# Kernel tuning notes

Hardware: AMD Instinct MI355X
Metric: run time of the kernel (lower is better)

## Reference

```python
import jax, jax.numpy as jnp
import numpy as np

RANK = 16
RATIO_1 = 0.01
RATIO_2 = 0.01
N_POWER_ITERS = 2  # randomized SVD power iterations (torch.svd_lowrank-style)


def _lowrank_V(A, rank, key):
    """Randomized low-rank right factor V (n, rank) of A (m, n), a la svd_lowrank."""
    m, n = A.shape
    omega = jax.random.normal(key, (n, rank), dtype=A.dtype)
    Q, _ = jnp.linalg.qr(A @ omega)              # (m, rank)
    for _ in range(N_POWER_ITERS):
        Z, _ = jnp.linalg.qr(A.T @ Q)            # (n, rank)
        Q, _ = jnp.linalg.qr(A @ Z)              # (m, rank)
    B = Q.T @ A                                  # (rank, n) small
    _, _, Vt = jnp.linalg.svd(B, full_matrices=False)
    return Vt.T                                  # (n, rank), orthonormal cols


def _get_statistics(x, ratio):
    # threshold such that ~ratio fraction of |x| entries are outliers
    return jnp.quantile(jnp.abs(x), 1.0 - ratio)


def _compress(x, thresh, rank, key):
    d = x.shape[-1]
    x2d = x.reshape(-1, d)                       # (M, D)
    outliers = jnp.where(jnp.abs(x2d) > thresh, x2d, jnp.zeros((), x2d.dtype))
    residual = x2d - outliers
    R = _lowrank_V(residual, rank, key)          # (D, rank)
    L = residual @ R                             # (M, rank)
    Rinv = R.T                                   # orthonormal cols -> pinv = R^T
    return outliers, L, R, Rinv


def reference(x1, x2):
    # Hadamard product (the module's returned value)
    result = x1 * x2
    # iteration == 0 path: compute statistics and run SVD compression
    out1 = _get_statistics(x1, RATIO_1)
    out2 = _get_statistics(x2, RATIO_2)
    k = jax.random.key(42)
    k1, k2 = jax.random.split(k)
    _, _, R1, Rinv1 = _compress(x1, out1, RANK, k1)
    _, _, R2, Rinv2 = _compress(x2, out2, RANK, k2)
    return (result, out1, R1, Rinv1, out2, R2, Rinv2)


def setup_inputs() -> dict:
    key = jax.random.key(0)
    k1, k2 = jax.random.split(key)
    x1 = jax.random.normal(k1, (4, 2048, 4096), dtype=jnp.float32)
    x2 = jax.random.normal(k2, (4, 2048, 4096), dtype=jnp.float32)
    return {"x1": x1, "x2": x2}
```

## Files before the change

kernel.cpp:

```cpp
#include <hip/hip_runtime.h>
#include <cstdint>
#include <cstddef>


#define DEV __device__ __forceinline__

typedef float nfloat4 __attribute__((ext_vector_type(4)));

constexpr long long NTOT = 33554432LL;
constexpr unsigned long long KSEL = 33218888ULL;
constexpr uint32_t WLO = 0x40100000u;

constexpr long long OUT_T1  = 33554432LL;
constexpr long long OUT_R1  = 33554433LL;
constexpr long long OUT_RI1 = 33619969LL;
constexpr long long OUT_T2  = 33685505LL;
constexpr long long OUT_R2  = 33685506LL;
constexpr long long OUT_RI2 = 33751042LL;

constexpr size_t OFF_WPART  = 0;
constexpr size_t OFF_BPART  = 0;
constexpr size_t OFF_FB     = 4194304;
constexpr size_t OFF_CNT    = 6291456;
constexpr size_t OFF_GF     = 6291472;
constexpr size_t ZERO_BASE  = OFF_FB;
constexpr size_t ZERO_FLOATS= 2099216;
constexpr size_t OFF_CHIST  = 6291456;
constexpr size_t OFF_COARSE = 8388608;
constexpr size_t OFF_SEGS   = 8392704;
constexpr size_t OFF_SELR   = 8394752;
constexpr size_t OFF_TSEL   = 8394768;
constexpr size_t OFF_OMT    = 8394784;
constexpr size_t OFF_BIGY   = 8525856;
constexpr size_t OFF_BIGQ   = 8788000;
constexpr size_t OFF_ZT     = 9050144;
constexpr size_t OFF_QQR    = 9181216;
constexpr size_t OFF_TMAT   = 9312288;
constexpr size_t OFF_GRAMP  = 9443360;
constexpr size_t OFF_S      = 9476128;
constexpr size_t OFF_QTOP   = 9476640;
constexpr size_t OFF_RG     = 9477152;
constexpr size_t OFF_VTL    = 9477664;

DEV float frcp_(float x){ return __builtin_amdgcn_rcpf(x); }
DEV float fdivf_(float a, float b){ return a * __builtin_amdgcn_rcpf(b); }
DEV float fsqrtf_(float x){ return __builtin_amdgcn_sqrtf(x); }

#define TFR(a,b,r) { a += b; b = (b << r) | (b >> (32 - r)); b ^= a; }

DEV void d_threefry(uint32_t k0, uint32_t k1, uint32_t x0, uint32_t x1,
                    uint32_t& o0, uint32_t& o1){
  uint32_t ks2 = k0 ^ k1 ^ 0x1BD11BDAu;
  x0 += k0; x1 += k1;
  TFR(x0,x1,13) TFR(x0,x1,15) TFR(x0,x1,26) TFR(x0,x1,6)
  x0 += k1; x1 += ks2 + 1u;
  TFR(x0,x1,17) TFR(x0,x1,29) TFR(x0,x1,16) TFR(x0,x1,24)
  x0 += ks2; x1 += k0 + 2u;
  TFR(x0,x1,13) TFR(x0,x1,15) TFR(x0,x1,26) TFR(x0,x1,6)
  x0 += k0; x1 += k1 + 3u;
  TFR(x0,x1,17) TFR(x0,x1,29) TFR(x0,x1,16) TFR(x0,x1,24)
  x0 += k1; x1 += ks2 + 4u;
  TFR(x0,x1,13) TFR(x0,x1,15) TFR(x0,x1,26) TFR(x0,x1,6)
  x0 += ks2; x1 += k0 + 5u;
  o0 = x0; o1 = x1;
}

static void h_threefry(uint32_t k0, uint32_t k1, uint32_t x0, uint32_t x1,
                       uint32_t& o0, uint32_t& o1){
  uint32_t ks2 = k0 ^ k1 ^ 0x1BD11BDAu;
  x0 += k0; x1 += k1;
  TFR(x0,x1,13) TFR(x0,x1,15) TFR(x0,x1,26) TFR(x0,x1,6)
  x0 += k1; x1 += ks2 + 1u;
  TFR(x0,x1,17) TFR(x0,x1,29) TFR(x0,x1,16) TFR(x0,x1,24)
  x0 += ks2; x1 += k0 + 2u;
  TFR(x0,x1,13) TFR(x0,x1,15) TFR(x0,x1,26) TFR(x0,x1,6)
  x0 += k0; x1 += k1 + 3u;
  TFR(x0,x1,17) TFR(x0,x1,29) TFR(x0,x1,16) TFR(x0,x1,24)
  x0 += k1; x1 += ks2 + 4u;
  TFR(x0,x1,13) TFR(x0,x1,15) TFR(x0,x1,26) TFR(x0,x1,6)
  x0 += ks2; x1 += k0 + 5u;
  o0 = x0; o1 = x1;
}

DEV float erfinv_f32(float x){
  float w = -log1pf(-x*x);
  float p;
  if (w < 5.0f){
    w -= 2.5f;
    p = 2.81022636e-08f;
    p = fmaf(p, w, 3.43273939e-07f);
    p = fmaf(p, w, -3.5233877e-06f);
    p = fmaf(p, w, -4.39150654e-06f);
    p = fmaf(p, w, 0.00021858087f);
    p = fmaf(p, w, -0.00125372503f);
    p = fmaf(p, w, -0.00417768164f);
    p = fmaf(p, w, 0.246640727f);
    p = fmaf(p, w, 1.50140941f);
  } else {
    w = sqrtf(w) - 3.0f;
    p = -0.000200214257f;
    p = fmaf(p, w, 0.000100950558f);
    p = fmaf(p, w, 0.00134934322f);
    p = fmaf(p, w, -0.00367342844f);
    p = fmaf(p, w, 0.00573950773f);
    p = fmaf(p, w, -0.0076224613f);
    p = fmaf(p, w, 0.00943887047f);
    p = fmaf(p, w, 1.00167406f);
    p = fmaf(p, w, 2.83297682f);
  }
  return p * x;
}

DEV float lapy2f(float x, float y){
  float xa = fabsf(x), ya = fabsf(y);
  float w = fmaxf(xa, ya), z = fminf(xa, ya);
  if (z == 0.f) return w;
  float q = z * frcp_(w);
  return w * fsqrtf_(1.f + q*q);
}

DEV void slartg_(float f, float g, float& c, float& s, float& r){
  if (g == 0.f){ c = 1.f; s = 0.f; r = f; }
  else if (f == 0.f){ c = 0.f; s = copysignf(1.f, g); r = fabsf(g); }
  else {
    float d = fsqrtf_(f*f + g*g);
    float rd = frcp_(d);
    c = fabsf(f) * rd;
    r = copysignf(d, f);
    s = g * copysignf(rd, f);
// ... 168 lines not shown
  ps[threadIdx.x] = s;
  __syncthreads();
  if (threadIdx.x == 0){
    unsigned long long K = KSEL, cum = cnt[ty];
    int valid = 0, sbin = 0, rank = 0;
    if (K >= cum){
      int g = 0;
      for (; g < 256; g++){ if (cum + ps[g] > K) break; cum += ps[g]; }
      if (g < 256){
        for (int j = 0; j < 8; j++){
          uint32_t c = H[g*8 + j];
          if (cum + c > K){ sbin = g*8 + j; rank = (int)(K - cum); valid = 1; break; }
          cum += c;
        }
      }
    }
    selr[0] = sbin; selr[1] = rank; selr[2] = valid;
  }
}

__global__ __launch_bounds__(256) void k_fine(const float* __restrict__ x1,
    const float* __restrict__ x2, float* __restrict__ ws){
  int ty = blockIdx.y;
  const int* selr = (const int*)(ws + OFF_SELR) + ty*4;
  if (!selr[2]) return;
  uint32_t g = (uint32_t)selr[0];
  __shared__ uint32_t lh[1024];
  for (int i = threadIdx.x; i < 1024; i += 256) lh[i] = 0u;
  __syncthreads();
  const float4* x4 = (const float4*)(ty ? x2 : x1);
  long long n4 = NTOT/4;
  long long stride = (long long)gridDim.x * 256;
  for (long long i = (long long)blockIdx.x*256 + threadIdx.x; i < n4; i += stride){
    float4 a = x4[i];
    uint32_t dd;
    dd = (__float_as_uint(a.x)&0x7fffffffu) - WLO;
    if ((dd>>10) == g) atomicAdd(&lh[dd & 1023u], 1u);
    dd = (__float_as_uint(a.y)&0x7fffffffu) - WLO;
    if ((dd>>10) == g) atomicAdd(&lh[dd & 1023u], 1u);
    dd = (__float_as_uint(a.z)&0x7fffffffu) - WLO;
    if ((dd>>10) == g) atomicAdd(&lh[dd & 1023u], 1u);
    dd = (__float_as_uint(a.w)&0x7fffffffu) - WLO;
    if ((dd>>10) == g) atomicAdd(&lh[dd & 1023u], 1u);
  }
  __syncthreads();
  uint32_t* gf = (uint32_t*)(ws + OFF_GF) + (size_t)ty*1024;
  for (int i = threadIdx.x; i < 1024; i += 256){
    uint32_t v = lh[i];
    if (v) atomicAdd(&gf[i], v);
  }
}

__global__ __launch_bounds__(256) void k_fine_sel(float* __restrict__ ws,
    float* __restrict__ out){
  int ty = blockIdx.x;
  const int* selr = (const int*)(ws + OFF_SELR) + ty*4;
  if (!selr[2]) return;
  const uint32_t* gf = (const uint32_t*)(ws + OFF_GF) + (size_t)ty*1024;
  __shared__ uint32_t sh[1024];
  __shared__ uint32_t ps[256];
  int t = threadIdx.x;
  for (int k = 0; k < 4; k++) sh[k*256 + t] = gf[k*256 + t];
  __syncthreads();
  ps[t] = sh[4*t] + sh[4*t+1] + sh[4*t+2] + sh[4*t+3];
  __syncthreads();
  if (t == 0){
    uint32_t K = (uint32_t)selr[1];
    uint32_t cum = 0; int q = 0;
    for (; q < 256; q++){ if (cum + ps[q] > K) break; cum += ps[q]; }
    if (q > 255) q = 255;
    int f = q*4 + 3;
    for (int jj = 0; jj < 4; jj++){
      uint32_t c = sh[q*4 + jj];
      if (cum + c > K){ f = q*4 + jj; break; }
      cum += c;
    }
    uint32_t bits = WLO + (((uint32_t)selr[0]) << 10) + (uint32_t)f;
    float th = __uint_as_float(bits);
    ws[OFF_TSEL + ty] = th;
    out[ty ? OUT_T2 : OUT_T1] = th;
  }
}

__global__ __launch_bounds__(256) void k_hist_fb(const float* __restrict__ x1,
    const float* __restrict__ x2, float* __restrict__ ws){
  const int* selr = (const int*)(ws + OFF_SELR);
  if (selr[2] && selr[4 + 2]) return;
  __shared__ uint32_t lh[2][4][2048];
  for (int i = threadIdx.x; i < 2*4*2048; i += 256) (&lh[0][0][0])[i] = 0u;
  __syncthreads();
  int rep = threadIdx.x & 3;
  const float4* a4 = (const float4*)x1;
  const float4* b4 = (const float4*)x2;
  long long n4 = NTOT/4;
  long long stride = (long long)gridDim.x * 256;
  for (long long i = (long long)blockIdx.x*256 + threadIdx.x; i < n4; i += stride){
    float4 a = a4[i], b = b4[i];
    uint32_t u;
    u = __float_as_uint(a.x)&0x7fffffffu; atomicAdd(&lh[0][rep][u>>20], 1u);
    u = __float_as_uint(a.y)&0x7fffffffu; atomicAdd(&lh[0][rep][u>>20], 1u);
    u = __float_as_uint(a.z)&0x7fffffffu; atomicAdd(&lh[0][rep][u>>20], 1u);
    u = __float_as_uint(a.w)&0x7fffffffu; atomicAdd(&lh[0][rep][u>>20], 1u);
    u = __float_as_uint(b.x)&0x7fffffffu; atomicAdd(&lh[1][rep][u>>20], 1u);
    u = __float_as_uint(b.y)&0x7fffffffu; atomicAdd(&lh[1][rep][u>>20], 1u);
    u = __float_as_uint(b.z)&0x7fffffffu; atomicAdd(&lh[1][rep][u>>20], 1u);
    u = __float_as_uint(b.w)&0x7fffffffu; atomicAdd(&lh[1][rep][u>>20], 1u);
  }
  __syncthreads();
  uint32_t* ch = (uint32_t*)(ws + OFF_CHIST);
  for (int i = threadIdx.x; i < 2048; i += 256){
    uint32_t c0 = lh[0][0][i] + lh[0][1][i] + lh[0][2][i] + lh[0][3][i];
    uint32_t c1 = lh[1][0][i] + lh[1][1][i] + lh[1][2][i] + lh[1][3][i];
    ch[((size_t)blockIdx.x*2 + 0)*2048 + i] = c0;
    ch[((size_t)blockIdx.x*2 + 1)*2048 + i] = c1;
  }
}

__global__ __launch_bounds__(256) void k_coarse_red(float* __restrict__ ws){
  int ty = blockIdx.y;
  if (((const int*)(ws + OFF_SELR))[ty*4 + 2]) return;
  const uint32_t* ch = (const uint32_t*)(ws + OFF_CHIST);
  uint32_t* h = (uint32_t*)(ws + OFF_COARSE) + ty*2048;
  int bin = blockIdx.x*128 + (threadIdx.x & 127);
  int half = threadIdx.x >> 7;
  uint32_t s = 0;
  for (int p = half*256; p < half*256 + 256; p++)
    s += ch[((size_t)p*2 + ty)*2048 + bin];
  __shared__ uint32_t sh[256];
  sh[threadIdx.x] = s;
  __syncthreads();
  if (threadIdx.x < 128) h[bin] = sh[threadIdx.x] + sh[threadIdx.x + 128];
}

__global__ __launch_bounds__(256) void k_coarse_scan(float* __restrict__ ws){
  int ty = blockIdx.x;
  int* selr = (int*)(ws + OFF_SELR) + ty*4;
  if (selr[2]) return;
  const uint32_t* h = (const uint32_t*)(ws + OFF_COARSE) + ty*2048;
  __shared__ unsigned long long ps[256];
  unsigned long long s = 0;
  for (int j = 0; j < 8; j++) s += h[threadIdx.x*8 + j];
  ps[threadIdx.x] = s;
  __syncthreads();
  if (threadIdx.x == 0){
    unsigned long long cum = 0, K = KSEL;
    int g = 0;
    for (; g < 256; g++){ if (cum + ps[g] > K) break; cum += ps[g]; }
    if (g > 255) g = 255;
    int bin = 2047;
    for (int j = 0; j < 8; j++){
      uint32_t c = h[g*8 + j];
      if (cum + c > K){ bin = g*8 + j; break; }
      cum += c;
    }
    selr[0] = bin;
    selr[1] = (int)(K - cum);
  }
}

__global__ __launch_bounds__(256) void k_fine_fb(const float* __restrict__ x1,
    const float* __restrict__ x2, float* __restrict__ ws){
  int ty = blockIdx.y;
  const int* selr = (const int*)(ws + OFF_SELR) + ty*4;
  if (selr[2]) return;
  const float4* x4 = (const float4*)(ty ? x2 : x1);
  uint32_t bin = (uint32_t)selr[0];
  uint32_t* f = (uint32_t*)(ws + OFF_FB) + ((size_t)ty<<20);
  long long n4 = NTOT/4;
  long long stride = (long long)gridDim.x * 256;
  for (long long i = (long long)blockIdx.x*256 + threadIdx.x; i < n4; i += stride){
    float4 a = x4[i];
    uint32_t u;
    u = __float_as_uint(a.x)&0x7fffffffu; if ((u>>20)==bin) atomicAdd(&f[u&0xFFFFFu],1u);
    u = __float_as_uint(a.y)&0x7fffffffu; if ((u>>20)==bin) atomicAdd(&f[u&0xFFFFFu],1u);
    u = __float_as_uint(a.z)&0x7fffffffu; if ((u>>20)==bin) atomicAdd(&f[u&0xFFFFFu],1u);
    u = __float_as_uint(a.w)&0x7fffffffu; if ((u>>20)==bin) atomicAdd(&f[u&0xFFFFFu],1u);
  }
}

__global__ __launch_bounds__(256) void k_seg_sum(float* __restrict__ ws){
  int ty = blockIdx.y;
  const int* selr = (const int*)(ws + OFF_SELR) + ty*4;
  if (selr[2]) return;
  const uint32_t* f = (const uint32_t*)(ws + OFF_FB) + ((size_t)ty<<20);
  uint32_t* segs = (uint32_t*)(ws + OFF_SEGS) + ty*1024;
  uint32_t s = 0;
  int base = blockIdx.x*1024;
  for (int k = 0; k < 4; k++) s += f[base + k*256 + threadIdx.x];
  __shared__ uint32_t sh[256];
  sh[threadIdx.x] = s;
  __syncthreads();
  for (int off = 128; off > 0; off >>= 1){
    if (threadIdx.x < off) sh[threadIdx.x] += sh[threadIdx.x + off];
    __syncthreads();
  }
  if (threadIdx.x == 0) segs[blockIdx.x] = sh[0];
}

__global__ __launch_bounds__(256) void k_fine_scan2(float* __restrict__ ws, float* __restrict__ out){
  int ty = blockIdx.x;
  const int* selr = (const int*)(ws + OFF_SELR) + ty*4;
  if (selr[2]) return;
  const uint32_t* f = (const uint32_t*)(ws + OFF_FB) + ((size_t)ty<<20);
  const uint32_t* segs = (const uint32_t*)(ws + OFF_SEGS) + ty*1024;
  __shared__ uint32_t sh[1024];
  __shared__ uint32_t ps[256];
  __shared__ int gsel; __shared__ uint32_t csel;
  int t = threadIdx.x;
  uint32_t K = (uint32_t)selr[1];
  for (int k = 0; k < 4; k++) sh[k*256 + t] = segs[k*256 + t];
  __syncthreads();
  ps[t] = sh[4*t] + sh[4*t+1] + sh[4*t+2] + sh[4*t+3];
  __syncthreads();
  if (t == 0){
    uint32_t cum = 0; int q = 0;
    for (; q < 256; q++){ if (cum + ps[q] > K) break; cum += ps[q]; }
    if (q > 255) q = 255;
    int g = q*4;
    for (int j = 0; j < 4; j++){
      uint32_t c = sh[q*4 + j];
      if (cum + c > K){ g = q*4 + j; break; }
      cum += c;
      if (j == 3) g = q*4 + 3;
    }
    gsel = g; csel = cum;
  }
  __syncthreads();
  int g = gsel;
  for (int k = 0; k < 4; k++) sh[k*256 + t] = f[(size_t)g*1024 + k*256 + t];
  __syncthreads();
  ps[t] = sh[4*t] + sh[4*t+1] + sh[4*t+2] + sh[4*t+3];
  __syncthreads();
  if (t == 0){
    uint32_t cum = csel; int q = 0;
    for (; q < 256; q++){ if (cum + ps[q] > K) break; cum += ps[q]; }
    if (q > 255) q = 255;
    int j = q*4 + 3;
    for (int jj = 0; jj < 4; jj++){
      uint32_t c = sh[q*4 + jj];
      if (cum + c > K){ j = q*4 + jj; break; }
      cum += c;
    }
    uint32_t bits = (((uint32_t)selr[0])<<20) | (uint32_t)((g*1024 + j) & 0xFFFFF);
    float th = __uint_as_float(bits);
    ws[OFF_TSEL + ty] = th;
    out[ty ? OUT_T2 : OUT_T1] = th;
  }
}

__global__ __launch_bounds__(256) void k_omega(uint32_t a0, uint32_t a1,
    uint32_t b0, uint32_t b1, float* __restrict__ ws){
  int ty = blockIdx.y;
  uint32_t k0 = ty ? b0 : a0, k1 = ty ? b1 : a1;
  int i = blockIdx.x*256 + threadIdx.x;
  uint32_t o0, o1;
  d_threefry(k0, k1, 0u, (uint32_t)i, o0, o1);
  uint32_t bits = o0 ^ o1;
  float fr = __uint_as_float((bits >> 9) | 0x3f800000u) - 1.0f;
  const float lo = -0.99999994f;
  float u = fr * 2.0f + lo;
  u = fmaxf(lo, u);
  float v = 1.41421356237f * erfinv_f32(u);
  int row = i >> 4, col = i & 15;
  ws[OFF_OMT + (size_t)ty*65536 + (size_t)col*4096 + row] = v;
}

__global__ __launch_bounds__(256) void k_atype(const float* __restrict__ x1,
    const float* __restrict__ x2, float* __restrict__ ws, size_t wtOff){
  int ty = blockIdx.y;
  const float* x = ty ? x2 : x1;
  const float* wt = ws + wtOff + (size_t)ty*65536;
  float* Y = ws + OFF_BIGY + (size_t)ty*131072;
  float t = ws[OFF_TSEL + ty];
  int wave = threadIdx.x >> 6, lane = threadIdx.x & 63;
  __shared__ __align__(16) float wts[16][256];
  __shared__ float outs[16][16];
  float acc[4][16];
  #pragma unroll
  for (int r = 0; r < 4; r++)
    #pragma unroll
    for (int j = 0; j < 16; j++) acc[r][j] = 0.f;
  int rowbase = blockIdx.x*16 + wave*4;
  for (int c = 0; c < 4096; c += 256){
    __syncthreads();
    for (int idx = threadIdx.x; idx < 16*64; idx += 256){
      int j = idx >> 6, q = idx & 63;
      ((float4*)&wts[j][0])[q] = ((const float4*)(wt + (size_t)j*4096 + c))[q];
    }
    __syncthreads();
    float4 xv[4];
    #pragma unroll
    for (int rr = 0; rr < 4; rr++){
      int row = rowbase + rr;
      float4 a = ((const float4*)(x + (size_t)row*4096 + c))[lane];
      a.x = fabsf(a.x) > t ? 0.f : a.x;
      a.y = fabsf(a.y) > t ? 0.f : a.y;
      a.z = fabsf(a.z) > t ? 0.f : a.z;
      a.w = fabsf(a.w) > t ? 0.f : a.w;
      xv[rr] = a;
    }
    #pragma unroll
    for (int j = 0; j < 16; j++){
      float4 w4 = ((const float4*)&wts[j][0])[lane];
      #pragma unroll
      for (int rr = 0; rr < 4; rr++){
        acc[rr][j] = fmaf(xv[rr].x, w4.x, acc[rr][j]);
        acc[rr][j] = fmaf(xv[rr].y, w4.y, acc[rr][j]);
        acc[rr][j] = fmaf(xv[rr].z, w4.z, acc[rr][j]);
        acc[rr][j] = fmaf(xv[rr].w, w4.w, acc[rr][j]);
      }
    }
  }
  #pragma unroll
  for (int rr = 0; rr < 4; rr++)
    for (int j = 0; j < 16; j++){
      float v = acc[rr][j];
      for (int off = 32; off > 0; off >>= 1) v += __shfl_xor(v, off, 64);
      if (lane == 0) outs[wave*4 + rr][j] = v;
    }
  __syncthreads();
  int r = threadIdx.x >> 4, cc = threadIdx.x & 15;
  Y[(size_t)(blockIdx.x*16 + r)*16 + cc] = outs[r][cc];
}

__global__ __launch_bounds__(256) void k_gramP(float* __restrict__ ws, size_t mOff,
    size_t mStr){
// ... 289 lines not shown
        w *= tv;
        A[i][jj] -= w;
        for (int r = i+1; r < n; r++) A[r][jj] -= w*A[r][i];
      }
      __syncthreads();
    }
    if (i < n-1){
      float alpha = A[i][i+1];
      float ssum = 0.f;
      for (int c = i+2; c < n; c++) ssum += A[i][c]*A[i][c];
      float xn = fsqrtf_(ssum);
      float beta, tp;
      if (n - i - 1 <= 1 || xn == 0.f){ tp = 0.f; beta = alpha; }
      else {
        beta = -copysignf(lapy2f(alpha, xn), alpha);
        tp = fdivf_(beta - alpha, beta);
        float sc = frcp_(alpha - beta);
        if (l >= i+2 && l < n) A[i][l] *= sc;
      }
      if (l == 0){ e_[i] = beta; taup[i] = tp; }
      __syncthreads();
      if (tp != 0.f && l > i && l < n){
        int r = l;
        float w = A[r][i+1];
        for (int c = i+2; c < n; c++) w += A[i][c]*A[r][c];
        w *= tp;
        A[r][i+1] -= w;
        for (int c = i+2; c < n; c++) A[r][c] -= w*A[i][c];
      }
      __syncthreads();
    } else {
      if (l == 0) taup[i] = 0.f;
      __syncthreads();
    }
  }
  float D[16], E[16], vt[16];
  #pragma unroll
  for (int k = 0; k < 16; k++){
    D[k] = d_[k];
    E[k] = (k < 15) ? e_[k] : 0.f;
    vt[k] = (k == l) ? 1.f : 0.f;
  }
  auto getD = [&](int i)->float{ float r = D[0];
    #pragma unroll
    for (int k = 1; k < 16; k++) if (i == k) r = D[k];
    return r; };
  auto setD = [&](int i, float v){
    #pragma unroll
    for (int k = 0; k < 16; k++) if (i == k) D[k] = v; };
  auto getE = [&](int i)->float{ float r = E[0];
    #pragma unroll
    for (int k = 1; k < 16; k++) if (i == k) r = E[k];
    return r; };
  auto setE = [&](int i, float v){
    #pragma unroll
    for (int k = 0; k < 16; k++) if (i == k) E[k] = v; };
  auto getVt = [&](int i)->float{ float r = vt[0];
    #pragma unroll
    for (int k = 1; k < 16; k++) if (i == k) r = vt[k];
    return r; };
  auto setVt = [&](int i, float v){
    #pragma unroll
    for (int k = 0; k < 16; k++) if (i == k) vt[k] = v; };

  const float eps = 5.9604645e-08f;
  const float unfl = 1.17549435e-38f;
  const float tol = 10.f*eps;
  float sminoa = fabsf(D[0]);
  if (sminoa != 0.f){
    float mu = sminoa;
    #pragma unroll
    for (int i = 1; i < 16; i++){
      mu = fabsf(D[i])*fdivf_(mu, mu + fabsf(E[i-1]));
      sminoa = fminf(sminoa, mu);
    }
  }
  sminoa = sminoa * 0.25f;
  float thresh = fmaxf(tol*sminoa, (float)(6*n*n)*unfl);
  int maxit = 6*n*n;
  int iter = 0, oldll = -1, oldm = -1, mm = n, idir = 0;
  while (true){
    if (mm <= 1) break;
    if (iter > maxit) break;
    float smaxw = fabsf(getD(mm-1));
    int llv = 1; bool split = false;
    {
      bool done = false;
      #pragma unroll
      for (int c = 14; c >= 0; c--){
        if (c <= mm-2 && !done){
          if (fabsf(E[c]) <= thresh){ split = true; llv = c+1; done = true; }
          else smaxw = fmaxf(smaxw, fmaxf(fabsf(D[c]), fabsf(E[c])));
        }
      }
    }
    if (split){
      setE(llv-1, 0.f);
      if (llv == mm-1){ mm = mm - 1; continue; }
      llv = llv + 1;
    }
    if (llv == mm-1){
      float sigmn, sigmx, sinr, cosr, sinl, cosl;
      slasv2_(getD(mm-2), getE(mm-2), getD(mm-1), sigmn, sigmx, sinr, cosr, sinl, cosl);
      setD(mm-2, sigmx); setE(mm-2, 0.f); setD(mm-1, sigmn);
      float t1 = getVt(mm-2), t2 = getVt(mm-1);
      setVt(mm-2, cosr*t1 + sinr*t2);
      setVt(mm-1, cosr*t2 - sinr*t1);
      mm -= 2;
      continue;
    }
    if (llv > oldm || mm < oldll)
      idir = (fabsf(getD(llv-1)) >= fabsf(getD(mm-1))) ? 1 : 2;
    bool deflated = false;
    float sminl = 0.f;
    if (idir == 1){
      if (fabsf(getE(mm-2)) <= tol*fabsf(getD(mm-1))){ setE(mm-2, 0.f); continue; }
      float mu = fabsf(getD(llv-1)); sminl = mu;
      #pragma unroll
      for (int c = 0; c < 15; c++){
        if (c >= llv-1 && c <= mm-2 && !deflated){
          if (fabsf(E[c]) <= tol*mu){ E[c] = 0.f; deflated = true; }
          else {
            mu = fabsf(D[c+1])*fdivf_(mu, mu + fabsf(E[c]));
            sminl = fminf(sminl, mu);
          }
        }
      }
    } else {
      if (fabsf(getE(llv-1)) <= tol*fabsf(getD(llv-1))){ setE(llv-1, 0.f); continue; }
      float mu = fabsf(getD(mm-1)); sminl = mu;
      #pragma unroll
      for (int c = 14; c >= 0; c--){
        if (c >= llv-1 && c <= mm-2 && !deflated){
          if (fabsf(E[c]) <= tol*mu){ E[c] = 0.f; deflated = true; }
          else {
            mu = fabsf(D[c])*fdivf_(mu, mu + fabsf(E[c]));
            sminl = fminf(sminl, mu);
          }
        }
      }
    }
    if (deflated) continue;
    oldll = llv; oldm = mm;
    float shift = 0.f, rdum;
    if (!((float)n*tol*fdivf_(sminl, smaxw) <= fmaxf(eps, 0.01f*tol))){
      float sll;
      if (idir == 1){ sll = fabsf(getD(llv-1)); slas2_(getD(mm-2), getE(mm-2), getD(mm-1), shift, rdum); }
      else          { sll = fabsf(getD(mm-1));  slas2_(getD(llv-1), getE(llv-1), getD(llv), shift, rdum); }
      if (sll > 0.f){ float q = fdivf_(shift, sll); if (q*q < eps) shift = 0.f; }
    }
    iter += mm - llv;
    if (shift == 0.f){
      if (idir == 1){
        float cs = 1.f, oldcs = 1.f, sn = 0.f, oldsn = 0.f, rr, dnew;
        #pragma unroll
        for (int i0 = 0; i0 < 15; i0++){
          if (i0 >= llv-1 && i0 <= mm-2){
            slartg_(D[i0]*cs, E[i0], cs, sn, rr);
            if (i0 > llv-1) E[i0-1 < 0 ? 0 : i0-1] = oldsn*rr;
            slartg_(oldcs*rr, D[i0+1]*sn, oldcs, oldsn, dnew);
            D[i0] = dnew;
            if (cs != 1.f || sn != 0.f){
              float t1 = vt[i0], t2 = vt[i0+1];
              vt[i0+1] = cs*t2 - sn*t1;
              vt[i0]   = sn*t2 + cs*t1;
            }
          }
        }
        float h = getD(mm-1)*cs;
        setD(mm-1, h*oldcs);
        float hv = h*oldsn;
        setE(mm-2, (fabsf(hv) <= thresh) ? 0.f : hv);
      } else {
        float cs = 1.f, oldcs = 1.f, sn = 0.f, oldsn = 0.f, rr, dnew;
        #pragma unroll
        for (int i0 = 15; i0 >= 1; i0--){
          if (i0 >= llv && i0 <= mm-1){
            slartg_(D[i0]*cs, E[i0-1], cs, sn, rr);
            if (i0 < mm-1) E[i0] = oldsn*rr;
            slartg_(oldcs*rr, D[i0-1]*sn, oldcs, oldsn, dnew);
            D[i0] = dnew;
            float cR = oldcs, sR = -oldsn;
            if (cR != 1.f || sR != 0.f){
              float t1 = vt[i0-1], t2 = vt[i0];
              vt[i0]   = cR*t2 - sR*t1;
              vt[i0-1] = sR*t2 + cR*t1;
            }
          }
        }
        float h = getD(llv-1)*cs;
        setD(llv-1, h*oldcs);
        float hv = h*oldsn;
        setE(llv-1, (fabsf(hv) <= thresh) ? 0.f : hv);
      }
    } else {
      if (idir == 1){
        float dl = getD(llv-1);
        float ff = (fabsf(dl) - shift)*(copysignf(1.f, dl) + fdivf_(shift, dl));
        float gg = getE(llv-1);
        float cosr, sinr, cosl, sinl, rr;
        #pragma unroll
        for (int i0 = 0; i0 < 15; i0++){
          if (i0 >= llv-1 && i0 <= mm-2){
            slartg_(ff, gg, cosr, sinr, rr);
            if (i0 > llv-1) E[i0-1 < 0 ? 0 : i0-1] = rr;
            float di = D[i0], ei = E[i0];
            ff = cosr*di + sinr*ei;
            E[i0] = cosr*ei - sinr*di;
            gg = sinr*D[i0+1];
            D[i0+1] = cosr*D[i0+1];
            slartg_(ff, gg, cosl, sinl, rr);
            D[i0] = rr;
            float ei2 = E[i0], dip = D[i0+1];
            ff = cosl*ei2 + sinl*dip;
            D[i0+1] = cosl*dip - sinl*ei2;
            if (i0 < mm-2){
              gg = sinl*E[i0+1];
              E[i0+1] = cosl*E[i0+1];
            }
            if (cosr != 1.f || sinr != 0.f){
              float t1 = vt[i0], t2 = vt[i0+1];
              vt[i0+1] = cosr*t2 - sinr*t1;
              vt[i0]   = sinr*t2 + cosr*t1;
            }
          }
        }
        setE(mm-2, (fabsf(ff) <= thresh) ? 0.f : ff);
      } else {
        float dm = getD(mm-1);
        float ff = (fabsf(dm) - shift)*(copysignf(1.f, dm) + fdivf_(shift, dm));
        float gg = getE(mm-2);
        float cosr, sinr, cosl, sinl, rr;
        #pragma unroll
        for (int i0 = 15; i0 >= 1; i0--){
          if (i0 >= llv && i0 <= mm-1){
            slartg_(ff, gg, cosr, sinr, rr);
            if (i0 < mm-1) E[i0] = rr;
            float di = D[i0], eim = E[i0-1];
            ff = cosr*di + sinr*eim;
            E[i0-1] = cosr*eim - sinr*di;
            gg = sinr*D[i0-1];
            D[i0-1] = cosr*D[i0-1];
            slartg_(ff, gg, cosl, sinl, rr);
            D[i0] = rr;
            float eim2 = E[i0-1], dim = D[i0-1];
            ff = cosl*eim2 + sinl*dim;
            D[i0-1] = cosl*dim - sinl*eim2;
            if (i0 > llv){
              gg = sinl*E[i0-2 < 0 ? 0 : i0-2];
              E[i0-2 < 0 ? 0 : i0-2] = cosl*E[i0-2 < 0 ? 0 : i0-2];
            }
            float cR = cosr, sR = -sinr;
            if (cR != 1.f || sR != 0.f){
              float t1 = vt[i0-1], t2 = vt[i0];
              vt[i0]   = cR*t2 - sR*t1;
              vt[i0-1] = sR*t2 + cR*t1;
            }
          }
        }
        setE(llv-1, (fabsf(ff) <= thresh) ? 0.f : ff);
      }
    }
  }
  #pragma unroll
  for (int k = 0; k < 16; k++){
    if (D[k] < 0.f){ D[k] = -D[k]; vt[k] = -vt[k]; }
  }
  #pragma unroll
  for (int i = 1; i <= 15; i++){
    int isub = 1; float smn = D[0];
    #pragma unroll
    for (int jj = 2; jj <= 16; jj++){
      if (jj <= 16 + 1 - i){
        if (D[jj-1] <= smn){ isub = jj; smn = D[jj-1]; }
      }
    }
    if (isub != 16 + 1 - i){
      setD(isub - 1, D[16 - i]);
      D[16 - i] = smn;
      float tmp = getVt(isub - 1);
      setVt(isub - 1, vt[16 - i]);
      vt[16 - i] = tmp;
    }
  }
  if (l < 16){
    #pragma unroll
    for (int r = 0; r < 16; r++) VTm[r][l] = vt[r];
  }
  __syncthreads();
  for (int i = n-2; i >= 0; i--){
    float tp = taup[i];
    if (tp != 0.f && l < 16){
      int r = l;
      float w = VTm[r][i+1];
      for (int c = i+2; c < n; c++) w += VTm[r][c]*A[i][c];
      w *= tp;
      VTm[r][i+1] -= w;
      for (int c = i+2; c < n; c++) VTm[r][c] -= w*A[i][c];
    }
    __syncthreads();
  }
  for (int idx = l; idx < 256; idx += 64) vtlOut[idx] = VTm[idx>>4][idx&15];
}

__global__ __launch_bounds__(256) void k_rout(float* __restrict__ ws, float* __restrict__ out){
  int ty = blockIdx.y;
  const float* Qq = ws + OFF_QQR + (size_t)ty*65536;
  const float* vtl = ws + OFF_VTL + ty*256;
  long long Roff  = ty ? OUT_R2  : OUT_R1;
  long long RIoff = ty ? OUT_RI2 : OUT_RI1;
  __shared__ float V[16][16];
  int t = threadIdx.x;
  V[t>>4][t&15] = vtl[t];
  __syncthreads();
  int row = blockIdx.x*256 + t;
  float mv[16];
  #pragma unroll
  for (int q = 0; q < 4; q++){
    float4 v = ((const float4*)(Qq + (size_t)row*16))[q];
    mv[q*4] = v.x; mv[q*4+1] = v.y; mv[q*4+2] = v.z; mv[q*4+3] = v.w;
  }
  #pragma unroll
  for (int j = 0; j < 16; j++){
    float s = 0.f;
    #pragma unroll
    for (int i = 0; i < 16; i++) s = fmaf(mv[i], V[j][i], s);
    out[Roff + (long long)row*16 + j] = s;
    out[RIoff + (long long)j*4096 + row] = s;
  }
}

extern "C" void kernel_launch(void* const* d_in, const int* in_sizes, int n_in,
                              void* d_out, int out_size, void* d_ws, size_t ws_size,
                              hipStream_t stream){
  const float* x1 = (const float*)d_in[0];
  const float* x2 = (const float*)d_in[1];
  float* out = (float*)d_out;
  float* ws = (float*)d_ws;
  (void)in_sizes; (void)n_in; (void)out_size; (void)ws_size;

  hipMemsetAsync(ws + ZERO_BASE, 0, ZERO_FLOATS*sizeof(float), stream);

  k_had<<<dim3(1024), 256, 0, stream>>>(x1, x2, out, ws);
  k_red<<<dim3(8, 2), 1024, 0, stream>>>(ws);
  k_wselect<<<dim3(2), 256, 0, stream>>>(ws);
  k_fine<<<dim3(1024, 2), 256, 0, stream>>>(x1, x2, ws);
  k_fine_sel<<<dim3(2), 256, 0, stream>>>(ws, out);
  k_hist_fb<<<dim3(512), 256, 0, stream>>>(x1, x2, ws);
  k_coarse_red<<<dim3(16, 2), 256, 0, stream>>>(ws);
  k_coarse_scan<<<dim3(2), 256, 0, stream>>>(ws);
  k_fine_fb<<<dim3(1024, 2), 256, 0, stream>>>(x1, x2, ws);
  k_seg_sum<<<dim3(1024, 2), 256, 0, stream>>>(ws);
  k_fine_scan2<<<dim3(2), 256, 0, stream>>>(ws, out);

  uint32_t a0, a1, b0, b1;
  h_threefry(0u, 42u, 0u, 0u, a0, a1);
  h_threefry(0u, 42u, 0u, 1u, b0, b1);
  k_omega<<<dim3(256, 2), 256, 0, stream>>>(a0, a1, b0, b1, ws);

  k_atype<<<dim3(512, 2), 256, 0, stream>>>(x1, x2, ws, OFF_OMT);
  k_gramP<<<dim3(64, 2), 256, 0, stream>>>(ws, OFF_BIGY, 131072);
  k_tiny<<<dim3(2), 64, 0, stream>>>(ws, OFF_BIGY, 131072);
  k_applyq<<<dim3(32, 2), 256, 0, stream>>>(ws, OFF_BIGY, 131072, OFF_BIGQ, 131072, 8192, 1, 0);
  k_btype<<<dim3(256, 2), 256, 0, stream>>>(x1, x2, ws);
  k_bredgram<<<dim3(64, 2), 256, 0, stream>>>(ws);
  k_tiny<<<dim3(2), 64, 0, stream>>>(ws, OFF_TMAT, 65536);
  k_applyq<<<dim3(16, 2), 256, 0, stream>>>(ws, OFF_TMAT, 65536, OFF_ZT, 65536, 4096, 0, 1);
  k_atype<<<dim3(512, 2), 256, 0, stream>>>(x1, x2, ws, OFF_ZT);
  k_gramP<<<dim3(64, 2), 256, 0, stream>>>(ws, OFF_BIGY, 131072);
  k_tiny<<<dim3(2), 64, 0, stream>>>(ws, OFF_BIGY, 131072);
  k_applyq<<<dim3(32, 2), 256, 0, stream>>>(ws, OFF_BIGY, 131072, OFF_BIGQ, 131072, 8192, 1, 0);
  k_btype<<<dim3(256, 2), 256, 0, stream>>>(x1, x2, ws);
  k_bredgram<<<dim3(64, 2), 256, 0, stream>>>(ws);
  k_tiny<<<dim3(2), 64, 0, stream>>>(ws, OFF_TMAT, 65536);
  k_applyq<<<dim3(16, 2), 256, 0, stream>>>(ws, OFF_TMAT, 65536, OFF_ZT, 65536, 4096, 0, 1);
  k_atype<<<dim3(512, 2), 256, 0, stream>>>(x1, x2, ws, OFF_ZT);
  k_gramP<<<dim3(64, 2), 256, 0, stream>>>(ws, OFF_BIGY, 131072);
  k_tiny<<<dim3(2), 64, 0, stream>>>(ws, OFF_BIGY, 131072);
  k_applyq<<<dim3(32, 2), 256, 0, stream>>>(ws, OFF_BIGY, 131072, OFF_BIGQ, 131072, 8192, 1, 0);
  k_btype<<<dim3(256, 2), 256, 0, stream>>>(x1, x2, ws);
  k_bredgram<<<dim3(64, 2), 256, 0, stream>>>(ws);
  k_tiny<<<dim3(2), 64, 0, stream>>>(ws, OFF_TMAT, 65536);
  k_applyq<<<dim3(16, 2), 256, 0, stream>>>(ws, OFF_TMAT, 65536, OFF_QQR, 65536, 4096, 1, 0);

  k_chain<<<dim3(2), 64, 0, stream>>>(ws);
  k_rout<<<dim3(16, 2), 256, 0, stream>>>(ws, out);
}
```

Measured before the change: 1.643 ms.

## Merge quantile fallback into one guarded kernel; make SVD branch conditions wave-uniform

Six fallback kernels for the exact quantile (histogram, reductions, fine histogram, segment sums, scans) are replaced by a single two-block kernel that runs only when the fast path flagged failure. Normally it exits at once, so the cost of launching six kernels is removed. If the fallback does run, it is now a very slow serial single-block pass. Separately, the bidiagonal SVD loop now uses readfirstlane on its branch conditions and loads some values once up front, so control flow stays wave-uniform and redundant dynamic-index lookups are avoided.

```diff
diff --git a/kernel.cpp b/kernel.cpp
--- a/kernel.cpp
+++ b/kernel.cpp
@@ -25,7 +25,6 @@
 constexpr size_t OFF_GF     = 6291472;
 constexpr size_t ZERO_BASE  = OFF_FB;
 constexpr size_t ZERO_FLOATS= 2099216;
-constexpr size_t OFF_CHIST  = 6291456;
 constexpr size_t OFF_COARSE = 8388608;
 constexpr size_t OFF_SEGS   = 8392704;
 constexpr size_t OFF_SELR   = 8394752;
@@ -45,6 +44,8 @@
 DEV float frcp_(float x){ return __builtin_amdgcn_rcpf(x); }
 DEV float fdivf_(float a, float b){ return a * __builtin_amdgcn_rcpf(b); }
 DEV float fsqrtf_(float x){ return __builtin_amdgcn_sqrtf(x); }
+DEV int rfl(int x){ return __builtin_amdgcn_readfirstlane(x); }
+DEV uint32_t rflu(uint32_t x){ return (uint32_t)__builtin_amdgcn_readfirstlane((int)x); }
 
 #define TFR(a,b,r) { a += b; b = (b << r) | (b >> (32 - r)); b ^= a; }
 
@@ -379,66 +380,32 @@
   }
 }
 
-__global__ __launch_bounds__(256) void k_hist_fb(const float* __restrict__ x1,
-    const float* __restrict__ x2, float* __restrict__ ws){
-  const int* selr = (const int*)(ws + OFF_SELR);
-  if (selr[2] && selr[4 + 2]) return;
-  __shared__ uint32_t lh[2][4][2048];
-  for (int i = threadIdx.x; i < 2*4*2048; i += 256) (&lh[0][0][0])[i] = 0u;
-  __syncthreads();
-  int rep = threadIdx.x & 3;
-  const float4* a4 = (const float4*)x1;
-  const float4* b4 = (const float4*)x2;
+__global__ __launch_bounds__(256) void k_fallback(const float* __restrict__ x1,
+    const float* __restrict__ x2, float* __restrict__ ws, float* __restrict__ out){
+  int ty = blockIdx.x;
+  const int* selr = (const int*)(ws + OFF_SELR) + ty*4;
+  if (selr[2]) return;
+  const float4* x4 = (const float4*)(ty ? x2 : x1);
   long long n4 = NTOT/4;
-  long long stride = (long long)gridDim.x * 256;
-  for (long long i = (long long)blockIdx.x*256 + threadIdx.x; i < n4; i += stride){
-    float4 a = a4[i], b = b4[i];
-    uint32_t u;
-    u = __float_as_uint(a.x)&0x7fffffffu; atomicAdd(&lh[0][rep][u>>20], 1u);
-    u = __float_as_uint(a.y)&0x7fffffffu; atomicAdd(&lh[0][rep][u>>20], 1u);
-    u = __float_as_uint(a.z)&0x7fffffffu; atomicAdd(&lh[0][rep][u>>20], 1u);
-    u = __float_as_uint(a.w)&0x7fffffffu; atomicAdd(&lh[0][rep][u>>20], 1u);
-    u = __float_as_uint(b.x)&0x7fffffffu; atomicAdd(&lh[1][rep][u>>20], 1u);
-    u = __float_as_uint(b.y)&0x7fffffffu; atomicAdd(&lh[1][rep][u>>20], 1u);
-    u = __float_as_uint(b.z)&0x7fffffffu; atomicAdd(&lh[1][rep][u>>20], 1u);
-    u = __float_as_uint(b.w)&0x7fffffffu; atomicAdd(&lh[1][rep][u>>20], 1u);
-  }
-  __syncthreads();
-  uint32_t* ch = (uint32_t*)(ws + OFF_CHIST);
-  for (int i = threadIdx.x; i < 2048; i += 256){
-    uint32_t c0 = lh[0][0][i] + lh[0][1][i] + lh[0][2][i] + lh[0][3][i];
-    uint32_t c1 = lh[1][0][i] + lh[1][1][i] + lh[1][2][i] + lh[1][3][i];
-    ch[((size_t)blockIdx.x*2 + 0)*2048 + i] = c0;
-    ch[((size_t)blockIdx.x*2 + 1)*2048 + i] = c1;
-  }
-}
-
-__global__ __launch_bounds__(256) void k_coarse_red(float* __restrict__ ws){
-  int ty = blockIdx.y;
-  if (((const int*)(ws + OFF_SELR))[ty*4 + 2]) return;
-  const uint32_t* ch = (const uint32_t*)(ws + OFF_CHIST);
-  uint32_t* h = (uint32_t*)(ws + OFF_COARSE) + ty*2048;
-  int bin = blockIdx.x*128 + (threadIdx.x & 127);
-  int half = threadIdx.x >> 7;
-  uint32_t s = 0;
-  for (int p = half*256; p < half*256 + 256; p++)
-    s += ch[((size_t)p*2 + ty)*2048 + bin];
-  __shared__ uint32_t sh[256];
-  sh[threadIdx.x] = s;
-  __syncthreads();
-  if (threadIdx.x < 128) h[bin] = sh[threadIdx.x] + sh[threadIdx.x + 128];
-}
-
-__global__ __launch_bounds__(256) void k_coarse_scan(float* __restrict__ ws){
-  int ty = blockIdx.x;
-  int* selr = (int*)(ws + OFF_SELR) + ty*4;
-  if (selr[2]) return;
-  const uint32_t* h = (const uint32_t*)(ws + OFF_COARSE) + ty*2048;
+  __shared__ uint32_t lh[2048];
+  for (int i = threadIdx.x; i < 2048; i += 256) lh[i] = 0u;
+  __syncthreads();
+  for (long long i = threadIdx.x; i < n4; i += 256){
+    float4 a = x4[i];
+    atomicAdd(&lh[(__float_as_uint(a.x)&0x7fffffffu)>>20], 1u);
+    atomicAdd(&lh[(__float_as_uint(a.y)&0x7fffffffu)>>20], 1u);
+    atomicAdd(&lh[(__float_as_uint(a.z)&0x7fffffffu)>>20], 1u);
+    atomicAdd(&lh[(__float_as_uint(a.w)&0x7fffffffu)>>20], 1u);
+  }
+  __syncthreads();
   __shared__ unsigned long long ps[256];
-  unsigned long long s = 0;
-  for (int j = 0; j < 8; j++) s += h[threadIdx.x*8 + j];
-  ps[threadIdx.x] = s;
-  __syncthreads();
+  {
+    unsigned long long s = 0;
+    for (int j = 0; j < 8; j++) s += lh[threadIdx.x*8 + j];
+    ps[threadIdx.x] = s;
+  }
+  __syncthreads();
+  __shared__ int sbin; __shared__ uint32_t srank;
   if (threadIdx.x == 0){
     unsigned long long cum = 0, K = KSEL;
     int g = 0;
@@ -446,26 +413,16 @@
     if (g > 255) g = 255;
     int bin = 2047;
     for (int j = 0; j < 8; j++){
-      uint32_t c = h[g*8 + j];
+      uint32_t c = lh[g*8 + j];
       if (cum + c > K){ bin = g*8 + j; break; }
       cum += c;
     }
-    selr[0] = bin;
-    selr[1] = (int)(K - cum);
-  }
-}
-
-__global__ __launch_bounds__(256) void k_fine_fb(const float* __restrict__ x1,
-    const float* __restrict__ x2, float* __restrict__ ws){
-  int ty = blockIdx.y;
-  const int* selr = (const int*)(ws + OFF_SELR) + ty*4;
-  if (selr[2]) return;
-  const float4* x4 = (const float4*)(ty ? x2 : x1);
-  uint32_t bin = (uint32_t)selr[0];
+    sbin = bin; srank = (uint32_t)(K - cum);
+  }
+  __syncthreads();
+  uint32_t bin = (uint32_t)sbin;
   uint32_t* f = (uint32_t*)(ws + OFF_FB) + ((size_t)ty<<20);
-  long long n4 = NTOT/4;
-  long long stride = (long long)gridDim.x * 256;
-  for (long long i = (long long)blockIdx.x*256 + threadIdx.x; i < n4; i += stride){
+  for (long long i = threadIdx.x; i < n4; i += 256){
     float4 a = x4[i];
     uint32_t u;
     u = __float_as_uint(a.x)&0x7fffffffu; if ((u>>20)==bin) atomicAdd(&f[u&0xFFFFFu],1u);
@@ -473,72 +430,37 @@
     u = __float_as_uint(a.z)&0x7fffffffu; if ((u>>20)==bin) atomicAdd(&f[u&0xFFFFFu],1u);
     u = __float_as_uint(a.w)&0x7fffffffu; if ((u>>20)==bin) atomicAdd(&f[u&0xFFFFFu],1u);
   }
-}
-
-__global__ __launch_bounds__(256) void k_seg_sum(float* __restrict__ ws){
-  int ty = blockIdx.y;
-  const int* selr = (const int*)(ws + OFF_SELR) + ty*4;
-  if (selr[2]) return;
-  const uint32_t* f = (const uint32_t*)(ws + OFF_FB) + ((size_t)ty<<20);
-  uint32_t* segs = (uint32_t*)(ws + OFF_SEGS) + ty*1024;
-  uint32_t s = 0;
-  int base = blockIdx.x*1024;
-  for (int k = 0; k < 4; k++) s += f[base + k*256 + threadIdx.x];
-  __shared__ uint32_t sh[256];
-  sh[threadIdx.x] = s;
-  __syncthreads();
-  for (int off = 128; off > 0; off >>= 1){
-    if (threadIdx.x < off) sh[threadIdx.x] += sh[threadIdx.x + off];
-    __syncthreads();
-  }
-  if (threadIdx.x == 0) segs[blockIdx.x] = sh[0];
-}
-
-__global__ __launch_bounds__(256) void k_fine_scan2(float* __restrict__ ws, float* __restrict__ out){
-  int ty = blockIdx.x;
-  const int* selr = (const int*)(ws + OFF_SELR) + ty*4;
-  if (selr[2]) return;
-  const uint32_t* f = (const uint32_t*)(ws + OFF_FB) + ((size_t)ty<<20);
-  const uint32_t* segs = (const uint32_t*)(ws + OFF_SEGS) + ty*1024;
-  __shared__ uint32_t sh[1024];
-  __shared__ uint32_t ps[256];
-  __shared__ int gsel; __shared__ uint32_t csel;
-  int t = threadIdx.x;
-  uint32_t K = (uint32_t)selr[1];
-  for (int k = 0; k < 4; k++) sh[k*256 + t] = segs[k*256 + t];
-  __syncthreads();
-  ps[t] = sh[4*t] + sh[4*t+1] + sh[4*t+2] + sh[4*t+3];
-  __syncthreads();
-  if (t == 0){
-    uint32_t cum = 0; int q = 0;
-    for (; q < 256; q++){ if (cum + ps[q] > K) break; cum += ps[q]; }
+  __threadfence();
+  __syncthreads();
+  __shared__ uint32_t segs[1024];
+  for (int sgi = threadIdx.x; sgi < 1024; sgi += 256){
+    uint32_t ss = 0;
+    for (int j = 0; j < 1024; j++) ss += f[(size_t)sgi*1024 + j];
+    segs[sgi] = ss;
+  }
+  __syncthreads();
+  if (threadIdx.x == 0){
+    uint32_t K = srank, cum = 0;
+    int q = 0;
+    for (; q < 256; q++){
+      uint32_t pq = segs[4*q] + segs[4*q+1] + segs[4*q+2] + segs[4*q+3];
+      if (cum + pq > K) break;
+      cum += pq;
+    }
     if (q > 255) q = 255;
-    int g = q*4;
+    int g = q*4 + 3;
     for (int j = 0; j < 4; j++){
-      uint32_t c = sh[q*4 + j];
+      uint32_t c = segs[q*4 + j];
       if (cum + c > K){ g = q*4 + j; break; }
       cum += c;
-      if (j == 3) g = q*4 + 3;
-    }
-    gsel = g; csel = cum;
-  }
-  __syncthreads();
-  int g = gsel;
-  for (int k = 0; k < 4; k++) sh[k*256 + t] = f[(size_t)g*1024 + k*256 + t];
-  __syncthreads();
-  ps[t] = sh[4*t] + sh[4*t+1] + sh[4*t+2] + sh[4*t+3];
-  __syncthreads();
-  if (t == 0){
-    uint32_t cum = csel; int q = 0;
-    for (; q < 256; q++){ if (cum + ps[q] > K) break; cum += ps[q]; }
-    if (q > 255) q = 255;
-    int j = q*4 + 3;
-    for (int jj = 0; jj < 4; jj++){
-      uint32_t c = sh[q*4 + jj];
-      if (cum + c > K){ j = q*4 + jj; break; }
+    }
+    int jf = 1023;
+    for (int j = 0; j < 1024; j++){
+      uint32_t c = f[(size_t)g*1024 + j];
+      if (cum + c > K){ jf = j; break; }
       cum += c;
     }
-    uint32_t bits = (((uint32_t)selr[0])<<20) | (uint32_t)((g*1024 + j) & 0xFFFFF);
+    uint32_t bits = (bin<<20) | (uint32_t)((g*1024 + jf) & 0xFFFFF);
     float th = __uint_as_float(bits);
     ws[OFF_TSEL + ty] = th;
     out[ty ? OUT_T2 : OUT_T1] = th;
@@ -994,40 +916,47 @@
   while (true){
     if (mm <= 1) break;
     if (iter > maxit) break;
-    float smaxw = fabsf(getD(mm-1));
-    int llv = 1; bool split = false;
-    {
-      bool done = false;
-      #pragma unroll
-      for (int c = 14; c >= 0; c--){
-        if (c <= mm-2 && !done){
-          if (fabsf(E[c]) <= thresh){ split = true; llv = c+1; done = true; }
-          else smaxw = fmaxf(smaxw, fmaxf(fabsf(D[c]), fabsf(E[c])));
-        }
-      }
-    }
+    uint32_t msk = 0u;
+    #pragma unroll
+    for (int c = 0; c < 15; c++) msk |= (fabsf(E[c]) <= thresh) ? (1u << c) : 0u;
+    msk &= (1u << (mm-1)) - 1u;
+    msk = rflu(msk);
+    int llv, clow; bool split;
+    if (msk){ int cmax = 31 - __clz((int)msk); split = true; llv = cmax + 1; clow = cmax + 1; }
+    else    { split = false; llv = 1; clow = 0; }
+    float dm1 = getD(mm-1);
+    float smaxw = fabsf(dm1);
+    #pragma unroll
+    for (int c = 0; c < 15; c++)
+      if (c >= clow && c <= mm-2) smaxw = fmaxf(smaxw, fmaxf(fabsf(D[c]), fabsf(E[c])));
     if (split){
       setE(llv-1, 0.f);
-      if (llv == mm-1){ mm = mm - 1; continue; }
+      if (llv == mm-1){ mm = rfl(mm - 1); continue; }
       llv = llv + 1;
     }
+    float dm2 = getD(mm-2);
+    float e_m2 = getE(mm-2);
+    float dll = getD(llv-1);
+    float e_ll = getE(llv-1);
     if (llv == mm-1){
       float sigmn, sigmx, sinr, cosr, sinl, cosl;
-      slasv2_(getD(mm-2), getE(mm-2), getD(mm-1), sigmn, sigmx, sinr, cosr, sinl, cosl);
+      slasv2_(dm2, e_m2, dm1, sigmn, sigmx, sinr, cosr, sinl, cosl);
       setD(mm-2, sigmx); setE(mm-2, 0.f); setD(mm-1, sigmn);
       float t1 = getVt(mm-2), t2 = getVt(mm-1);
       setVt(mm-2, cosr*t1 + sinr*t2);
       setVt(mm-1, cosr*t2 - sinr*t1);
-      mm -= 2;
+      mm = rfl(mm - 2);
       continue;
     }
     if (llv > oldm || mm < oldll)
-      idir = (fabsf(getD(llv-1)) >= fabsf(getD(mm-1))) ? 1 : 2;
+      idir = (fabsf(dll) >= fabsf(dm1)) ? 1 : 2;
+    idir = rfl(idir);
     bool deflated = false;
     float sminl = 0.f;
     if (idir == 1){
-      if (fabsf(getE(mm-2)) <= tol*fabsf(getD(mm-1))){ setE(mm-2, 0.f); continue; }
-      float mu = fabsf(getD(llv-1)); sminl = mu;
+      int pc = (fabsf(e_m2) <= tol*fabsf(dm1)) ? 1 : 0;
+      if (rfl(pc)){ setE(mm-2, 0.f); continue; }
+      float mu = fabsf(dll); sminl = mu;
       #pragma unroll
       for (int c = 0; c < 15; c++){
         if (c >= llv-1 && c <= mm-2 && !deflated){
@@ -1039,8 +968,9 @@
         }
       }
     } else {
-      if (fabsf(getE(llv-1)) <= tol*fabsf(getD(llv-1))){ setE(llv-1, 0.f); continue; }
-      float mu = fabsf(getD(mm-1)); sminl = mu;
+      int pc = (fabsf(e_ll) <= tol*fabsf(dll)) ? 1 : 0;
+      if (rfl(pc)){ setE(llv-1, 0.f); continue; }
+      float mu = fabsf(dm1); sminl = mu;
       #pragma unroll
       for (int c = 14; c >= 0; c--){
         if (c >= llv-1 && c <= mm-2 && !deflated){
@@ -1052,17 +982,24 @@
         }
       }
     }
-    if (deflated) continue;
+    {
+      int dfl = deflated ? 1 : 0;
+      if (rfl(dfl)) continue;
+    }
     oldll = llv; oldm = mm;
     float shift = 0.f, rdum;
-    if (!((float)n*tol*fdivf_(sminl, smaxw) <= fmaxf(eps, 0.01f*tol))){
-      float sll;
-      if (idir == 1){ sll = fabsf(getD(llv-1)); slas2_(getD(mm-2), getE(mm-2), getD(mm-1), shift, rdum); }
-      else          { sll = fabsf(getD(mm-1));  slas2_(getD(llv-1), getE(llv-1), getD(llv), shift, rdum); }
-      if (sll > 0.f){ float q = fdivf_(shift, sll); if (q*q < eps) shift = 0.f; }
+    {
+      int nosh = (!((float)n*tol*fdivf_(sminl, smaxw) <= fmaxf(eps, 0.01f*tol))) ? 1 : 0;
+      if (rfl(nosh)){
+        float sll;
+        if (idir == 1){ sll = fabsf(dll); slas2_(dm2, e_m2, dm1, shift, rdum); }
+        else          { sll = fabsf(dm1); slas2_(dll, e_ll, getD(llv), shift, rdum); }
+        if (sll > 0.f){ float q = fdivf_(shift, sll); if (q*q < eps) shift = 0.f; }
+      }
     }
     iter += mm - llv;
-    if (shift == 0.f){
+    int zsh = (shift == 0.f) ? 1 : 0;
+    if (rfl(zsh)){
       if (idir == 1){
         float cs = 1.f, oldcs = 1.f, sn = 0.f, oldsn = 0.f, rr, dnew;
         #pragma unroll
@@ -1079,7 +1016,7 @@
             }
           }
         }
-        float h = getD(mm-1)*cs;
+        float h = dm1*cs;
         setD(mm-1, h*oldcs);
         float hv = h*oldsn;
         setE(mm-2, (fabsf(hv) <= thresh) ? 0.f : hv);
@@ -1100,16 +1037,16 @@
             }
           }
         }
-        float h = getD(llv-1)*cs;
+        float h = dll*cs;
         setD(llv-1, h*oldcs);
         float hv = h*oldsn;
         setE(llv-1, (fabsf(hv) <= thresh) ? 0.f : hv);
       }
     } else {
       if (idir == 1){
-        float dl = getD(llv-1);
+        float dl = dll;
         float ff = (fabsf(dl) - shift)*(copysignf(1.f, dl) + fdivf_(shift, dl));
-        float gg = getE(llv-1);
+        float gg = e_ll;
         float cosr, sinr, cosl, sinl, rr;
         #pragma unroll
         for (int i0 = 0; i0 < 15; i0++){
@@ -1139,9 +1076,9 @@
         }
         setE(mm-2, (fabsf(ff) <= thresh) ? 0.f : ff);
       } else {
-        float dm = getD(mm-1);
+        float dm = dm1;
         float ff = (fabsf(dm) - shift)*(copysignf(1.f, dm) + fdivf_(shift, dm));
-        float gg = getE(mm-2);
+        float gg = e_m2;
         float cosr, sinr, cosl, sinl, rr;
         #pragma unroll
         for (int i0 = 15; i0 >= 1; i0--){
@@ -1258,12 +1195,7 @@
   k_wselect<<<dim3(2), 256, 0, stream>>>(ws);
   k_fine<<<dim3(1024, 2), 256, 0, stream>>>(x1, x2, ws);
   k_fine_sel<<<dim3(2), 256, 0, stream>>>(ws, out);
-  k_hist_fb<<<dim3(512), 256, 0, stream>>>(x1, x2, ws);
-  k_coarse_red<<<dim3(16, 2), 256, 0, stream>>>(ws);
-  k_coarse_scan<<<dim3(2), 256, 0, stream>>>(ws);
-  k_fine_fb<<<dim3(1024, 2), 256, 0, stream>>>(x1, x2, ws);
-  k_seg_sum<<<dim3(1024, 2), 256, 0, stream>>>(ws);
-  k_fine_scan2<<<dim3(2), 256, 0, stream>>>(ws, out);
+  k_fallback<<<dim3(2), 256, 0, stream>>>(x1, x2, ws, out);
 
   uint32_t a0, a1, b0, b1;
   h_threefry(0u, 42u, 0u, 0u, a0, a1);
```

Measured after the change: 1.611 ms. -2.0%, faster.
